# Kernel tuning notes

Measured on AMD Instinct MI355X. Metric: run time of the kernel, lower is better.

The kernel has to match this reference:

```python
import jax, jax.numpy as jnp
import numpy as np

C, HEADS, H, W = 256, 8, 64, 64
HD = C // HEADS
EPS = 1e-5

def conv1x1(x, w, b):
    # x:[B,C,H,W], w:[O,C], b:[O]
    return jnp.einsum('bchw,oc->bohw', x, w) + b[None, :, None, None]

def group_norm(x, scale, bias):
    B = x.shape[0]
    xg = x.reshape(B, HEADS, HD, H, W)
    mu = jnp.mean(xg, axis=(2, 3, 4), keepdims=True)
    var = jnp.var(xg, axis=(2, 3, 4), keepdims=True)
    xn = ((xg - mu) * jax.lax.rsqrt(var + EPS)).reshape(B, C, H, W)
    return xn * scale[None, :, None, None] + bias[None, :, None, None]

def setup_inputs() -> dict:
    key = jax.random.key(0)
    ks = jax.random.split(key, 12)
    s = 1.0 / np.sqrt(C)
    d = {
        'x': jax.random.normal(ks[0], (1, C, H, W), jnp.float32),
        'wq': jax.random.normal(ks[1], (C, C), jnp.float32) * s,
        'bq': jax.random.normal(ks[2], (C,), jnp.float32) * 0.01,
        'wk': jax.random.normal(ks[3], (C, C), jnp.float32) * s,
        'bk': jax.random.normal(ks[4], (C,), jnp.float32) * 0.01,
        'wv': jax.random.normal(ks[5], (C, C), jnp.float32) * s,
        'bv': jax.random.normal(ks[6], (C,), jnp.float32) * 0.01,
        'wo': jax.random.normal(ks[7], (C, C), jnp.float32) * s,
        'bo': jax.random.normal(ks[8], (C,), jnp.float32) * 0.01,
        'gn_scale': jnp.ones((C,), jnp.float32),
        'gn_bias': jnp.zeros((C,), jnp.float32),
        'gamma': jax.random.normal(ks[9], (1,), jnp.float32) * 0.1,
    }
    return d

def reference(x, wq, bq, wk, bk, wv, bv, wo, bo, gn_scale, gn_bias, gamma):
    B = x.shape[0]
    N = H * W
    scale = HD ** (-0.5)
    xn = group_norm(x, gn_scale, gn_bias)
    q = conv1x1(xn, wq, bq).reshape(B, HEADS, HD, N)
    k = conv1x1(xn, wk, bk).reshape(B, HEADS, HD, N)
    v = conv1x1(xn, wv, bv).reshape(B, HEADS, HD, N)
    attn = jnp.einsum('bhdn,bhdm->bhnm', q, k) * scale  # [B,h,N,N]
    attn = jax.nn.softmax(attn, axis=-1)
    out = jnp.einsum('bhnm,bhdm->bhdn', attn, v).reshape(B, C, H, W)
    out = conv1x1(out, wo, bo)
    return x + gamma * out
```

## Files before the change

kernel.cpp:

```cpp
#include <hip/hip_runtime.h>
#include <hip/hip_bf16.h>

#define C_DIM 256
#define N_SP  4096
#define HEADS 8
#define HD    32
#define GSIZE (HD * N_SP)

typedef __attribute__((ext_vector_type(8))) short bf16x8;
typedef __attribute__((ext_vector_type(4))) float f32x4;
typedef __attribute__((ext_vector_type(4))) unsigned u32x4;

__device__ inline unsigned short f2bf(float f) {
  unsigned int u = __builtin_bit_cast(unsigned int, f);
  u = (u + 0x7fffu + ((u >> 16) & 1u)) >> 16;
  return (unsigned short)u;
}
__device__ inline float bf2f(unsigned short b) {
  return __builtin_bit_cast(float, (unsigned)b << 16);
}

__device__ inline unsigned cvtpk_bf16(float lo, float hi) {
  unsigned r;
  asm("v_cvt_pk_bf16_f32 %0, %1, %2" : "=v"(r) : "v"(lo), "v"(hi));
  return r;
}
__device__ inline void pl32swap(unsigned &x, unsigned &y) {
  asm("v_permlane32_swap_b32 %0, %1" : "+v"(x), "+v"(y));
}
__device__ inline void pl16swap(unsigned &x, unsigned &y) {
  asm("v_permlane16_swap_b32 %0, %1" : "+v"(x), "+v"(y));
}
__device__ inline void gload_lds16(const void* g, void* l) {
  __builtin_amdgcn_global_load_lds(
      (const __attribute__((address_space(1))) void*)g,
      (__attribute__((address_space(3))) void*)l, 16, 0, 0);
}

__global__ __launch_bounds__(1024) void stats_cvt(const float* __restrict__ x,
                                                  float* __restrict__ pstats,
                                                  const float* __restrict__ wq,
                                                  const float* __restrict__ wk,
                                                  const float* __restrict__ wv,
                                                  const float* __restrict__ wo,
                                                  unsigned short* __restrict__ dst) {
  int t = threadIdx.x;
  if (blockIdx.x < 64) {
    int g = blockIdx.x >> 3, sub = blockIdx.x & 7;
    const float4* xg = reinterpret_cast<const float4*>(
        x + (size_t)g * GSIZE + (size_t)sub * (GSIZE / 8));
    float s1 = 0.f, s2 = 0.f;
#pragma unroll
    for (int i = 0; i < 4; ++i) {
      float4 v = xg[t + i * 1024];
      s1 += v.x + v.y + v.z + v.w;
      s2 += v.x * v.x + v.y * v.y + v.z * v.z + v.w * v.w;
    }
    for (int off = 1; off < 64; off <<= 1) {
      s1 += __shfl_xor(s1, off);
      s2 += __shfl_xor(s2, off);
    }
    __shared__ float red[16][2];
    int wid = t >> 6;
    if ((t & 63) == 0) { red[wid][0] = s1; red[wid][1] = s2; }
    __syncthreads();
    if (t < 16) {
      s1 = red[t][0]; s2 = red[t][1];
      for (int off = 1; off < 16; off <<= 1) {
        s1 += __shfl_xor(s1, off);
        s2 += __shfl_xor(s2, off);
      }
      if (t == 0) {
        pstats[(g * 8 + sub) * 2] = s1;
        pstats[(g * 8 + sub) * 2 + 1] = s2;
      }
    }
  } else {
    int i = (blockIdx.x - 64) * 1024 + t;
    int mat = i >> 14;
    int idx = i & 16383;
    const float* src = (mat == 0) ? wq : (mat == 1) ? wk : (mat == 2) ? wv : wo;
    float4 v = reinterpret_cast<const float4*>(src)[idx];
    ushort4 o;
    o.x = f2bf(v.x); o.y = f2bf(v.y); o.z = f2bf(v.z); o.w = f2bf(v.w);
    reinterpret_cast<ushort4*>(dst + (size_t)mat * 65536)[idx] = o;
  }
}

__global__ __launch_bounds__(256) void gn_apply_t(const float* __restrict__ x,
                                                  const float* __restrict__ pstats,
                                                  const float* __restrict__ gsc,
                                                  const float* __restrict__ gbi,
                                                  unsigned short* __restrict__ xnt) {
  __shared__ float tile[64][65];
  __shared__ float gs[2][2];
  int t = threadIdx.x;
  int p0 = blockIdx.x * 64;
  int c0 = blockIdx.y * 64;
  if (t < 2) {
    int g = (c0 >> 5) + t;
    float s1 = 0.f, s2 = 0.f;
#pragma unroll
    for (int s = 0; s < 8; ++s) {
      s1 += pstats[(g * 8 + s) * 2];
      s2 += pstats[(g * 8 + s) * 2 + 1];
    }
    float mu = s1 / (float)GSIZE;
    float var = s2 / (float)GSIZE - mu * mu;
    gs[t][0] = mu;
    gs[t][1] = rsqrtf(var + 1e-5f);
  }
  __syncthreads();
#pragma unroll
  for (int pass = 0; pass < 4; ++pass) {
    int f = t + pass * 256;
    int row = f >> 4, f4 = f & 15;
    int c = c0 + row;
    float4 v = *reinterpret_cast<const float4*>(x + (size_t)c * N_SP + p0 + f4 * 4);
    float mu = gs[row >> 5][0], rs = gs[row >> 5][1];
    float sc = gsc[c] * rs;
    float bi = gbi[c] - mu * sc;
    tile[row][f4 * 4 + 0] = v.x * sc + bi;
    tile[row][f4 * 4 + 1] = v.y * sc + bi;
    tile[row][f4 * 4 + 2] = v.z * sc + bi;
    tile[row][f4 * 4 + 3] = v.w * sc + bi;
  }
  __syncthreads();
#pragma unroll
  for (int pass = 0; pass < 4; ++pass) {
    int f = t + pass * 256;
    int p = f >> 4, cg = f & 15;
    ushort4 o;
    o.x = f2bf(tile[cg * 4 + 0][p]);
    o.y = f2bf(tile[cg * 4 + 1][p]);
    o.z = f2bf(tile[cg * 4 + 2][p]);
    o.w = f2bf(tile[cg * 4 + 3][p]);
    *reinterpret_cast<ushort4*>(xnt + (size_t)(p0 + p) * C_DIM + c0 + cg * 4) = o;
  }
}

__global__ __launch_bounds__(256) void gemm_qkv(const unsigned short* __restrict__ xnt,
                                                const unsigned short* __restrict__ wbf,
                                                const float* __restrict__ bq,
                                                const float* __restrict__ bk,
                                                const float* __restrict__ bv,
                                                unsigned short* __restrict__ qt,
                                                unsigned short* __restrict__ kt,
                                                unsigned short* __restrict__ vv) {
  int t = threadIdx.x;
  int w = t >> 6, lc = t & 15, lg = (t & 63) >> 4;
  int z = blockIdx.y;
  const unsigned short* Wb = wbf + (size_t)z * 65536;

  if (z < 2) {
    const float* bias = (z == 0) ? bq : bk;
    unsigned short* outt = (z == 0) ? qt : kt;
    float scale = (z == 0) ? 0.25503344494963116f : 1.0f;
    int n_base = (blockIdx.x >> 1) * 32 + (w >> 1) * 16;
    int o_base = (blockIdx.x & 1) * 128 + (w & 1) * 64;
    f32x4 acc[4];
#pragma unroll
    for (int ni = 0; ni < 4; ++ni) acc[ni] = (f32x4){0.f, 0.f, 0.f, 0.f};
#pragma unroll
    for (int c0 = 0; c0 < 256; c0 += 32) {
      bf16x8 a = *reinterpret_cast<const bf16x8*>(
          xnt + (size_t)(n_base + lc) * C_DIM + c0 + 8 * lg);
#pragma unroll
      for (int ni = 0; ni < 4; ++ni) {
        bf16x8 b = *reinterpret_cast<const bf16x8*>(
            Wb + (size_t)(o_base + 16 * ni + lc) * C_DIM + c0 + 8 * lg);
        acc[ni] = __builtin_amdgcn_mfma_f32_16x16x32_bf16(a, b, acc[ni], 0, 0, 0);
      }
    }
#pragma unroll
    for (int ni = 0; ni < 4; ++ni) {
      float bvv = bias[o_base + 16 * ni + lc];
#pragma unroll
      for (int r = 0; r < 4; ++r)
        outt[(size_t)(n_base + 4 * lg + r) * C_DIM + o_base + 16 * ni + lc] =
            f2bf((acc[ni][r] + bvv) * scale);
    }
  } else {
    int o_base = (blockIdx.x >> 6) * 64 + (w >> 1) * 32;
    int p_base = (blockIdx.x & 63) * 64 + (w & 1) * 32;
    f32x4 acc[2][2];
#pragma unroll
    for (int mi = 0; mi < 2; ++mi)
#pragma unroll
      for (int ni = 0; ni < 2; ++ni) acc[mi][ni] = (f32x4){0.f, 0.f, 0.f, 0.f};
#pragma unroll
    for (int c0 = 0; c0 < 256; c0 += 32) {
      bf16x8 a[2], b[2];
#pragma unroll
      for (int mi = 0; mi < 2; ++mi)
        a[mi] = *reinterpret_cast<const bf16x8*>(
            Wb + (size_t)(o_base + 16 * mi + lc) * C_DIM + c0 + 8 * lg);
#pragma unroll
      for (int ni = 0; ni < 2; ++ni)
        b[ni] = *reinterpret_cast<const bf16x8*>(
            xnt + (size_t)(p_base + 16 * ni + lc) * C_DIM + c0 + 8 * lg);
#pragma unroll
      for (int mi = 0; mi < 2; ++mi)
#pragma unroll
        for (int ni = 0; ni < 2; ++ni)
          acc[mi][ni] = __builtin_amdgcn_mfma_f32_16x16x32_bf16(a[mi], b[ni], acc[mi][ni], 0, 0, 0);
    }
#pragma unroll
    for (int mi = 0; mi < 2; ++mi)
#pragma unroll
      for (int r = 0; r < 4; ++r) {
        int o = o_base + 16 * mi + 4 * lg + r;
        float bvv = bv[o];
#pragma unroll
        for (int ni = 0; ni < 2; ++ni)
          vv[(size_t)o * N_SP + p_base + 16 * ni + lc] = f2bf(acc[mi][ni][r] + bvv);
      }
  }
}


#define STAGE_Q(BB, IT)                                                       \
  {                                                                           \
    _Pragma("unroll")                                                         \
    for (int st = 0; st < 4; ++st) {                                          \
      gload_lds16(ksrc + (size_t)(IT) * 131072 + st * 32768,                  \
                  smem + (BB) + st * 4096 + w1024);                           \
      gload_lds16(vsrc + (size_t)(IT) * 512 + st * 128,                       \
                  smem + (BB) + 16384 + st * 4096 + w1024);                   \
    }                                                                         \
  }

#define CHAIN(KF, VF)                                                         \
  {                                                                           \
    f32x4 s[4];                                                               \
    _Pragma("unroll")                                                         \
    for (int ni = 0; ni < 4; ++ni) {                                          \
      f32x4 z = (f32x4){0.f, 0.f, 0.f, 0.f};                                  \
      s[ni] = __builtin_amdgcn_mfma_f32_16x16x32_bf16(KF[ni], qf[qi], z, 0, 0, 0); \
    }                                                                         \
    unsigned wd[4][2];                                                        \
    _Pragma("unroll")                                                         \
    for (int ni = 0; ni < 4; ++ni) {                                          \
      float p0 = __builtin_amdgcn_exp2f(s[ni][0]);                            \
      float p1 = __builtin_amdgcn_exp2f(s[ni][1]);                            \
      float p2 = __builtin_amdgcn_exp2f(s[ni][2]);                            \
      float p3 = __builtin_amdgcn_exp2f(s[ni][3]);                            \
      wd[ni][0] = cvtpk_bf16(p0, p1);                                         \
      wd[ni][1] = cvtpk_bf16(p2, p3);                                         \
    }                                                                         \
    bf16x8 ap[2];                                                             \
    _Pragma("unroll")                                                         \
    for (int kk = 0; kk < 2; ++kk) {                                          \
      unsigned a0 = wd[2 * kk][0], b0 = wd[2 * kk + 1][0];                    \
      unsigned a1 = wd[2 * kk][1], b1 = wd[2 * kk + 1][1];                    \
      pl32swap(a0, b0); pl16swap(a0, b0);                                     \
      pl32swap(a1, b1); pl16swap(a1, b1);                                     \
      u32x4 pk = {a0, a1, b0, b1};                                            \
      ap[kk] = __builtin_bit_cast(bf16x8, pk);                                \
    }                                                                         \
    lacc[qi] = __builtin_amdgcn_mfma_f32_16x16x32_bf16(ap[0], ones, lacc[qi], 0, 0, 0); \
    oacc[qi][0] = __builtin_amdgcn_mfma_f32_16x16x32_bf16(ap[0], VF[0][0], oacc[qi][0], 0, 0, 0); \
    oacc[qi][1] = __builtin_amdgcn_mfma_f32_16x16x32_bf16(ap[0], VF[0][1], oacc[qi][1], 0, 0, 0); \
    lacc[qi] = __builtin_amdgcn_mfma_f32_16x16x32_bf16(ap[1], ones, lacc[qi], 0, 0, 0); \
    oacc[qi][0] = __builtin_amdgcn_mfma_f32_16x16x32_bf16(ap[1], VF[1][0], oacc[qi][0], 0, 0, 0); \
    oacc[qi][1] = __builtin_amdgcn_mfma_f32_16x16x32_bf16(ap[1], VF[1][1], oacc[qi][1], 0, 0, 0); \
  }

#define COMPUTE_PAIR(BB, KOFF)                                                \
  {                                                                           \
    bf16x8 kf0[4], kf1[4], vf0[2][2], vf1[2][2];                              \
    _Pragma("unroll")                                                         \
    for (int ni = 0; ni < 4; ++ni) {                                          \
      kf0[ni] = *reinterpret_cast<const bf16x8*>(smem + (BB) + (KOFF) + ni * 1024 + krd); \
      kf1[ni] = *reinterpret_cast<const bf16x8*>(smem + (BB) + (KOFF) + 4096 + ni * 1024 + krd); \
    }                                                                         \
    _Pragma("unroll")                                                         \
    for (int dd = 0; dd < 2; ++dd) {                                          \
      vf0[0][dd] = *reinterpret_cast<const bf16x8*>(smem + (BB) + 16384 + (KOFF) + dd * 2048 + vrd0); \
      vf0[1][dd] = *reinterpret_cast<const bf16x8*>(smem + (BB) + 16384 + (KOFF) + dd * 2048 + vrd1); \
      vf1[0][dd] = *reinterpret_cast<const bf16x8*>(smem + (BB) + 16384 + (KOFF) + 4096 + dd * 2048 + vrd0); \
      vf1[1][dd] = *reinterpret_cast<const bf16x8*>(smem + (BB) + 16384 + (KOFF) + 4096 + dd * 2048 + vrd1); \
    }                                                                         \
    _Pragma("unroll")                                                         \
    for (int qi = 0; qi < 4; ++qi) {                                          \
      CHAIN(kf0, vf0)                                                         \
      CHAIN(kf1, vf1)                                                         \
    }                                                                         \
  }

#define SYNC_T                                                                \
  {                                                                           \
    asm volatile("s_waitcnt vmcnt(0)" ::: "memory");                          \
    __syncthreads();                                                          \
  }

__global__ __launch_bounds__(256, 2) void attn_part(const unsigned short* __restrict__ qt,
                                                    const unsigned short* __restrict__ kt,
                                                    const unsigned short* __restrict__ v,
                                                    unsigned short* __restrict__ po,
                                                    float* __restrict__ lp) {
  __shared__ __align__(1024) char smem[65536];
  int t = threadIdx.x;
  int w = t >> 6, lane = t & 63, lc = t & 15, lg = (t & 63) >> 4;
  int h = blockIdx.y, ks = blockIdx.z;
  int hc = h * HD;
  int nq0 = blockIdx.x * 256 + w * 64;
  int w1024 = w << 10;

  int kg = 64 * w + lane;
  int krow = kg >> 2;
  int kc16 = (kg & 3) ^ (krow & 3);
  const char* ksrc = (const char*)(kt + (size_t)(ks * 1024 + krow) * C_DIM + hc + 8 * kc16);
  int vg = 64 * w + lane;
  int vrow = vg >> 3;
  int vn16 = (vg & 7) ^ (vrow & 7);
  const char* vsrc = (const char*)(v + (size_t)(hc + vrow) * N_SP + ks * 1024 + 8 * vn16);

  int krd = lc * 64 + 16 * (lg ^ (lc & 3));
  int vrd0 = lc * 128 + 16 * ((lg + 0) ^ (lc & 7));
  int vrd1 = lc * 128 + 16 * ((lg + 4) ^ (lc & 7));

  bf16x8 qf[4];
#pragma unroll
  for (int qi = 0; qi < 4; ++qi)
    qf[qi] = *reinterpret_cast<const bf16x8*>(
        qt + (size_t)(nq0 + 16 * qi + lc) * C_DIM + hc + 8 * lg);

  f32x4 oacc[4][2], lacc[4];
#pragma unroll
  for (int qi = 0; qi < 4; ++qi) {
    lacc[qi] = (f32x4){0.f, 0.f, 0.f, 0.f};
#pragma unroll
    for (int dd = 0; dd < 2; ++dd) oacc[qi][dd] = (f32x4){0.f, 0.f, 0.f, 0.f};
  }
  const bf16x8 ones = {0x3F80, 0x3F80, 0x3F80, 0x3F80, 0x3F80, 0x3F80, 0x3F80, 0x3F80};

  STAGE_Q(0, 0)
  SYNC_T
  STAGE_Q(32768, 1)
  COMPUTE_PAIR(0, 0)
  COMPUTE_PAIR(0, 8192)
  SYNC_T
  STAGE_Q(0, 2)
  COMPUTE_PAIR(32768, 0)
  COMPUTE_PAIR(32768, 8192)
  SYNC_T
  STAGE_Q(32768, 3)
  COMPUTE_PAIR(0, 0)
  COMPUTE_PAIR(0, 8192)
  SYNC_T
  COMPUTE_PAIR(32768, 0)
  COMPUTE_PAIR(32768, 8192)

  unsigned short* pob = po + (size_t)ks * (N_SP * C_DIM);
#pragma unroll
  for (int qi = 0; qi < 4; ++qi)
#pragma unroll
    for (int dd = 0; dd < 2; ++dd)
#pragma unroll
      for (int r = 0; r < 4; ++r)
        pob[(size_t)(nq0 + 16 * qi + 4 * lg + r) * C_DIM + hc + 16 * dd + lc] =
            f2bf(oacc[qi][dd][r]);
  if (lc == 0) {
#pragma unroll
    for (int qi = 0; qi < 4; ++qi)
#pragma unroll
      for (int r = 0; r < 4; ++r)
        lp[ks * 32768 + h * N_SP + nq0 + 16 * qi + 4 * lg + r] = lacc[qi][r];
  }
}

__global__ __launch_bounds__(256) void attn_merge(const unsigned short* __restrict__ po,
                                                  const float* __restrict__ lp,
                                                  unsigned short* __restrict__ aot) {
  int i = blockIdx.x * 256 + threadIdx.x;
  int n = i >> 5;
  int c0 = (i & 31) * 8;
  int h = c0 >> 5;
  float l = lp[h * N_SP + n] + lp[32768 + h * N_SP + n] +
            lp[65536 + h * N_SP + n] + lp[98304 + h * N_SP + n];
  float rl = 1.0f / l;
  float acc[8] = {0.f, 0.f, 0.f, 0.f, 0.f, 0.f, 0.f, 0.f};
#pragma unroll
  for (int ksplit = 0; ksplit < 4; ++ksplit) {
    bf16x8 vv = *reinterpret_cast<const bf16x8*>(po + (size_t)ksplit * (N_SP * C_DIM) + (size_t)i * 8);
#pragma unroll
    for (int j = 0; j < 8; ++j) acc[j] += bf2f((unsigned short)vv[j]);
  }
  bf16x8 o;
#pragma unroll
  for (int j = 0; j < 8; ++j) o[j] = (short)f2bf(acc[j] * rl);
  *reinterpret_cast<bf16x8*>(aot + (size_t)i * 8) = o;
}

__global__ __launch_bounds__(256) void gemm_out(const unsigned short* __restrict__ Wb,
                                                const unsigned short* __restrict__ aot,
                                                const float* __restrict__ bias,
                                                const float* __restrict__ x,
                                                const float* __restrict__ gamma,
                                                float* __restrict__ out) {
  int t = threadIdx.x;
  int w = t >> 6, lc = t & 15, lg = (t & 63) >> 4;
  int o_base = blockIdx.y * 64 + (w >> 1) * 32;
  int p_base = blockIdx.x * 64 + (w & 1) * 32;
  f32x4 acc[2][2];
#pragma unroll
  for (int mi = 0; mi < 2; ++mi)
#pragma unroll
    for (int ni = 0; ni < 2; ++ni) acc[mi][ni] = (f32x4){0.f, 0.f, 0.f, 0.f};
#pragma unroll
  for (int c0 = 0; c0 < 256; c0 += 32) {
    bf16x8 a[2], b[2];
#pragma unroll
    for (int mi = 0; mi < 2; ++mi)
      a[mi] = *reinterpret_cast<const bf16x8*>(
          Wb + (size_t)(o_base + 16 * mi + lc) * C_DIM + c0 + 8 * lg);
#pragma unroll
    for (int ni = 0; ni < 2; ++ni)
      b[ni] = *reinterpret_cast<const bf16x8*>(
          aot + (size_t)(p_base + 16 * ni + lc) * C_DIM + c0 + 8 * lg);
#pragma unroll
    for (int mi = 0; mi < 2; ++mi)
#pragma unroll
      for (int ni = 0; ni < 2; ++ni)
        acc[mi][ni] = __builtin_amdgcn_mfma_f32_16x16x32_bf16(a[mi], b[ni], acc[mi][ni], 0, 0, 0);
  }
  float g = gamma[0];
#pragma unroll
  for (int mi = 0; mi < 2; ++mi)
#pragma unroll
    for (int r = 0; r < 4; ++r) {
      int o = o_base + 16 * mi + 4 * lg + r;
      float bvv = bias[o];
#pragma unroll
      for (int ni = 0; ni < 2; ++ni) {
        size_t idx = (size_t)o * N_SP + p_base + 16 * ni + lc;
        out[idx] = x[idx] + g * (acc[mi][ni][r] + bvv);
      }
    }
}

extern "C" void kernel_launch(void* const* d_in, const int* in_sizes, int n_in,
                              void* d_out, int out_size, void* d_ws, size_t ws_size,
                              hipStream_t stream) {
  const float* x   = (const float*)d_in[0];
  const float* wq  = (const float*)d_in[1];
  const float* bq  = (const float*)d_in[2];
  const float* wk  = (const float*)d_in[3];
  const float* bk  = (const float*)d_in[4];
  const float* wv  = (const float*)d_in[5];
  const float* bv  = (const float*)d_in[6];
  const float* wo  = (const float*)d_in[7];
  const float* bo  = (const float*)d_in[8];
  const float* gsc = (const float*)d_in[9];
  const float* gbi = (const float*)d_in[10];
  const float* gamma = (const float*)d_in[11];
  float* out = (float*)d_out;

  char* ws = (char*)d_ws;
  float* pstats         = (float*)(ws + 256);
  unsigned short* wbf   = (unsigned short*)(ws + 1024);
  unsigned short* qt    = (unsigned short*)(ws + 525312);
  unsigned short* kt    = (unsigned short*)(ws + 2622464);
  unsigned short* vv    = (unsigned short*)(ws + 4719616);
  unsigned short* aot   = (unsigned short*)(ws + 6816768);
  float* lp             = (float*)(ws + 8913920);
  unsigned short* xnt   = (unsigned short*)(ws + 9962496);
  unsigned short* po    = (unsigned short*)(ws + 12059648);

  stats_cvt<<<128, 1024, 0, stream>>>(x, pstats, wq, wk, wv, wo, wbf);
  gn_apply_t<<<dim3(64, 4), 256, 0, stream>>>(x, pstats, gsc, gbi, xnt);
  gemm_qkv<<<dim3(256, 3), 256, 0, stream>>>(xnt, wbf, bq, bk, bv, qt, kt, vv);
  attn_part<<<dim3(16, 8, 4), 256, 0, stream>>>(qt, kt, vv, po, lp);
  attn_merge<<<512, 256, 0, stream>>>(po, lp, aot);
  gemm_out<<<dim3(64, 4), 256, 0, stream>>>(wbf + 3 * 65536, aot, bo, x, gamma, out);
}
```

Before: 66.59 us.

## Fuse group-norm apply into QKV projection via shared-memory tile

Merges the group-norm apply kernel and the QKV GEMM into one kernel. Each block normalizes a 16-pixel by 256-channel slice of x into a bf16 LDS tile and computes Q, K and V for half of the output channels from it. This removes the xnt round trip through global memory and one kernel launch. In exchange, each block recomputes the normalization for its pixels (done twice, once per output half), the x loads are scalar strided reads rather than float4, and the GEMM tiles are smaller, giving less weight reuse per block.

```diff
diff --git a/kernel.cpp b/kernel.cpp
--- a/kernel.cpp
+++ b/kernel.cpp
@@ -87,18 +87,27 @@
   }
 }
 
-__global__ __launch_bounds__(256) void gn_apply_t(const float* __restrict__ x,
-                                                  const float* __restrict__ pstats,
-                                                  const float* __restrict__ gsc,
-                                                  const float* __restrict__ gbi,
-                                                  unsigned short* __restrict__ xnt) {
-  __shared__ float tile[64][65];
-  __shared__ float gs[2][2];
+__global__ __launch_bounds__(256) void gn_qkv(const float* __restrict__ x,
+                                              const float* __restrict__ pstats,
+                                              const float* __restrict__ gsc,
+                                              const float* __restrict__ gbi,
+                                              const unsigned short* __restrict__ wbf,
+                                              const float* __restrict__ bq,
+                                              const float* __restrict__ bk,
+                                              const float* __restrict__ bv,
+                                              unsigned short* __restrict__ qt,
+                                              unsigned short* __restrict__ kt,
+                                              unsigned short* __restrict__ vv) {
+  __shared__ unsigned short xt[16][264];
   int t = threadIdx.x;
-  int p0 = blockIdx.x * 64;
-  int c0 = blockIdx.y * 64;
-  if (t < 2) {
-    int g = (c0 >> 5) + t;
+  int p0 = (blockIdx.x >> 1) * 16;
+  int oh = (blockIdx.x & 1) * 128;
+
+  {
+    int pl = t & 15;
+    int cb = t >> 4;
+    int c0 = cb * 16;
+    int g = c0 >> 5;
     float s1 = 0.f, s2 = 0.f;
 #pragma unroll
     for (int s = 0; s < 8; ++s) {
@@ -106,116 +115,57 @@
       s2 += pstats[(g * 8 + s) * 2 + 1];
     }
     float mu = s1 / (float)GSIZE;
-    float var = s2 / (float)GSIZE - mu * mu;
-    gs[t][0] = mu;
-    gs[t][1] = rsqrtf(var + 1e-5f);
+    float rs = rsqrtf(s2 / (float)GSIZE - mu * mu + 1e-5f);
+#pragma unroll
+    for (int j = 0; j < 16; ++j) {
+      float sc = gsc[c0 + j] * rs;
+      float bi = gbi[c0 + j] - mu * sc;
+      xt[pl][c0 + j] = f2bf(x[(size_t)(c0 + j) * N_SP + p0 + pl] * sc + bi);
+    }
   }
   __syncthreads();
-#pragma unroll
-  for (int pass = 0; pass < 4; ++pass) {
-    int f = t + pass * 256;
-    int row = f >> 4, f4 = f & 15;
-    int c = c0 + row;
-    float4 v = *reinterpret_cast<const float4*>(x + (size_t)c * N_SP + p0 + f4 * 4);
-    float mu = gs[row >> 5][0], rs = gs[row >> 5][1];
-    float sc = gsc[c] * rs;
-    float bi = gbi[c] - mu * sc;
-    tile[row][f4 * 4 + 0] = v.x * sc + bi;
-    tile[row][f4 * 4 + 1] = v.y * sc + bi;
-    tile[row][f4 * 4 + 2] = v.z * sc + bi;
-    tile[row][f4 * 4 + 3] = v.w * sc + bi;
-  }
-  __syncthreads();
-#pragma unroll
-  for (int pass = 0; pass < 4; ++pass) {
-    int f = t + pass * 256;
-    int p = f >> 4, cg = f & 15;
-    ushort4 o;
-    o.x = f2bf(tile[cg * 4 + 0][p]);
-    o.y = f2bf(tile[cg * 4 + 1][p]);
-    o.z = f2bf(tile[cg * 4 + 2][p]);
-    o.w = f2bf(tile[cg * 4 + 3][p]);
-    *reinterpret_cast<ushort4*>(xnt + (size_t)(p0 + p) * C_DIM + c0 + cg * 4) = o;
-  }
-}
-
-__global__ __launch_bounds__(256) void gemm_qkv(const unsigned short* __restrict__ xnt,
-                                                const unsigned short* __restrict__ wbf,
-                                                const float* __restrict__ bq,
-                                                const float* __restrict__ bk,
-                                                const float* __restrict__ bv,
-                                                unsigned short* __restrict__ qt,
-                                                unsigned short* __restrict__ kt,
-                                                unsigned short* __restrict__ vv) {
-  int t = threadIdx.x;
+
   int w = t >> 6, lc = t & 15, lg = (t & 63) >> 4;
-  int z = blockIdx.y;
-  const unsigned short* Wb = wbf + (size_t)z * 65536;
-
-  if (z < 2) {
-    const float* bias = (z == 0) ? bq : bk;
-    unsigned short* outt = (z == 0) ? qt : kt;
-    float scale = (z == 0) ? 0.25503344494963116f : 1.0f;
-    int n_base = (blockIdx.x >> 1) * 32 + (w >> 1) * 16;
-    int o_base = (blockIdx.x & 1) * 128 + (w & 1) * 64;
-    f32x4 acc[4];
-#pragma unroll
-    for (int ni = 0; ni < 4; ++ni) acc[ni] = (f32x4){0.f, 0.f, 0.f, 0.f};
-#pragma unroll
-    for (int c0 = 0; c0 < 256; c0 += 32) {
-      bf16x8 a = *reinterpret_cast<const bf16x8*>(
-          xnt + (size_t)(n_base + lc) * C_DIM + c0 + 8 * lg);
-#pragma unroll
-      for (int ni = 0; ni < 4; ++ni) {
-        bf16x8 b = *reinterpret_cast<const bf16x8*>(
-            Wb + (size_t)(o_base + 16 * ni + lc) * C_DIM + c0 + 8 * lg);
-        acc[ni] = __builtin_amdgcn_mfma_f32_16x16x32_bf16(a, b, acc[ni], 0, 0, 0);
-      }
-    }
-#pragma unroll
-    for (int ni = 0; ni < 4; ++ni) {
-      float bvv = bias[o_base + 16 * ni + lc];
-#pragma unroll
-      for (int r = 0; r < 4; ++r)
-        outt[(size_t)(n_base + 4 * lg + r) * C_DIM + o_base + 16 * ni + lc] =
-            f2bf((acc[ni][r] + bvv) * scale);
-    }
-  } else {
-    int o_base = (blockIdx.x >> 6) * 64 + (w >> 1) * 32;
-    int p_base = (blockIdx.x & 63) * 64 + (w & 1) * 32;
-    f32x4 acc[2][2];
-#pragma unroll
-    for (int mi = 0; mi < 2; ++mi)
-#pragma unroll
-      for (int ni = 0; ni < 2; ++ni) acc[mi][ni] = (f32x4){0.f, 0.f, 0.f, 0.f};
-#pragma unroll
-    for (int c0 = 0; c0 < 256; c0 += 32) {
-      bf16x8 a[2], b[2];
-#pragma unroll
-      for (int mi = 0; mi < 2; ++mi)
-        a[mi] = *reinterpret_cast<const bf16x8*>(
-            Wb + (size_t)(o_base + 16 * mi + lc) * C_DIM + c0 + 8 * lg);
-#pragma unroll
-      for (int ni = 0; ni < 2; ++ni)
-        b[ni] = *reinterpret_cast<const bf16x8*>(
-            xnt + (size_t)(p_base + 16 * ni + lc) * C_DIM + c0 + 8 * lg);
-#pragma unroll
-      for (int mi = 0; mi < 2; ++mi)
-#pragma unroll
-        for (int ni = 0; ni < 2; ++ni)
-          acc[mi][ni] = __builtin_amdgcn_mfma_f32_16x16x32_bf16(a[mi], b[ni], acc[mi][ni], 0, 0, 0);
-    }
-#pragma unroll
-    for (int mi = 0; mi < 2; ++mi)
-#pragma unroll
-      for (int r = 0; r < 4; ++r) {
-        int o = o_base + 16 * mi + 4 * lg + r;
-        float bvv = bv[o];
-#pragma unroll
-        for (int ni = 0; ni < 2; ++ni)
-          vv[(size_t)o * N_SP + p_base + 16 * ni + lc] = f2bf(acc[mi][ni][r] + bvv);
-      }
-  }
+  int ow = oh + w * 32;
+  f32x4 aq[2], ak[2], av[2];
+#pragma unroll
+  for (int i = 0; i < 2; ++i) {
+    aq[i] = (f32x4){0.f, 0.f, 0.f, 0.f};
+    ak[i] = (f32x4){0.f, 0.f, 0.f, 0.f};
+    av[i] = (f32x4){0.f, 0.f, 0.f, 0.f};
+  }
+#pragma unroll
+  for (int it = 0; it < 8; ++it) {
+    bf16x8 a = *reinterpret_cast<const bf16x8*>(&xt[lc][it * 32 + 8 * lg]);
+#pragma unroll
+    for (int ni = 0; ni < 2; ++ni) {
+      size_t rowoff = (size_t)(ow + 16 * ni + lc) * C_DIM + it * 32 + 8 * lg;
+      bf16x8 bQ = *reinterpret_cast<const bf16x8*>(wbf + rowoff);
+      bf16x8 bK = *reinterpret_cast<const bf16x8*>(wbf + 65536 + rowoff);
+      bf16x8 bV = *reinterpret_cast<const bf16x8*>(wbf + 131072 + rowoff);
+      aq[ni] = __builtin_amdgcn_mfma_f32_16x16x32_bf16(a, bQ, aq[ni], 0, 0, 0);
+      ak[ni] = __builtin_amdgcn_mfma_f32_16x16x32_bf16(a, bK, ak[ni], 0, 0, 0);
+      av[ni] = __builtin_amdgcn_mfma_f32_16x16x32_bf16(bV, a, av[ni], 0, 0, 0);
+    }
+  }
+#pragma unroll
+  for (int ni = 0; ni < 2; ++ni) {
+    int o = ow + 16 * ni + lc;
+    float bqv = bq[o], bkv = bk[o];
+#pragma unroll
+    for (int r = 0; r < 4; ++r) {
+      qt[(size_t)(p0 + 4 * lg + r) * C_DIM + o] =
+          f2bf((aq[ni][r] + bqv) * 0.25503344494963116f);
+      kt[(size_t)(p0 + 4 * lg + r) * C_DIM + o] = f2bf(ak[ni][r] + bkv);
+    }
+  }
+#pragma unroll
+  for (int mi = 0; mi < 2; ++mi)
+#pragma unroll
+    for (int r = 0; r < 4; ++r) {
+      int o = ow + 16 * mi + 4 * lg + r;
+      vv[(size_t)o * N_SP + p0 + lc] = f2bf(av[mi][r] + bv[o]);
+    }
 }
 
 
@@ -241,12 +191,12 @@
     unsigned wd[4][2];                                                        \
     _Pragma("unroll")                                                         \
     for (int ni = 0; ni < 4; ++ni) {                                          \
-      float p0 = __builtin_amdgcn_exp2f(s[ni][0]);                            \
-      float p1 = __builtin_amdgcn_exp2f(s[ni][1]);                            \
-      float p2 = __builtin_amdgcn_exp2f(s[ni][2]);                            \
-      float p3 = __builtin_amdgcn_exp2f(s[ni][3]);                            \
-      wd[ni][0] = cvtpk_bf16(p0, p1);                                         \
-      wd[ni][1] = cvtpk_bf16(p2, p3);                                         \
+      float p0e = __builtin_amdgcn_exp2f(s[ni][0]);                           \
+      float p1e = __builtin_amdgcn_exp2f(s[ni][1]);                           \
+      float p2e = __builtin_amdgcn_exp2f(s[ni][2]);                           \
+      float p3e = __builtin_amdgcn_exp2f(s[ni][3]);                           \
+      wd[ni][0] = cvtpk_bf16(p0e, p1e);                                       \
+      wd[ni][1] = cvtpk_bf16(p2e, p3e);                                       \
     }                                                                         \
     bf16x8 ap[2];                                                             \
     _Pragma("unroll")                                                         \
@@ -465,12 +415,10 @@
   unsigned short* vv    = (unsigned short*)(ws + 4719616);
   unsigned short* aot   = (unsigned short*)(ws + 6816768);
   float* lp             = (float*)(ws + 8913920);
-  unsigned short* xnt   = (unsigned short*)(ws + 9962496);
   unsigned short* po    = (unsigned short*)(ws + 12059648);
 
   stats_cvt<<<128, 1024, 0, stream>>>(x, pstats, wq, wk, wv, wo, wbf);
-  gn_apply_t<<<dim3(64, 4), 256, 0, stream>>>(x, pstats, gsc, gbi, xnt);
-  gemm_qkv<<<dim3(256, 3), 256, 0, stream>>>(xnt, wbf, bq, bk, bv, qt, kt, vv);
+  gn_qkv<<<512, 256, 0, stream>>>(x, pstats, gsc, gbi, wbf, bq, bk, bv, qt, kt, vv);
   attn_part<<<dim3(16, 8, 4), 256, 0, stream>>>(qt, kt, vv, po, lp);
   attn_merge<<<512, 256, 0, stream>>>(po, lp, aot);
   gemm_out<<<dim3(64, 4), 256, 0, stream>>>(wbf + 3 * 65536, aot, bo, x, gamma, out);
```

New measurement: 63.72 us. -4.3%, faster.
